# Kernel tuning notes

Measured on AMD Instinct MI355X. Metric: run time of the kernel, lower is better.

## Reference

```python
import jax, jax.numpy as jnp
import numpy as np

UP = 2
KSIZE = 3
RES = 64
LRELU_SLOPE = 0.2
ACT_GAIN = float(np.sqrt(2.0))  # def_gain of 'lrelu' in bias_act


def _setup_filter():
    # upfirdn2d.setup_filter([1,3,3,1]): normalize, make separable 2D filter
    f = jnp.array([1.0, 3.0, 3.0, 1.0], dtype=jnp.float32)
    f = f / jnp.sum(f)
    return jnp.outer(f, f)  # [4,4]


def _upfirdn2d_up2(x, f2):
    # Zero-insertion upsample by 2 + pad + FIR filter, gain = up**2.
    # Torch path: zero-insert to 2H, pad (3,2), conv 4-tap -> 2H+2.
    # lhs_dilation gives 2H-1; absorbing the trailing inserted zero into the
    # right pad ((3,3) instead of (3,2)) is exactly equivalent.
    B, C, H, W = x.shape
    k = (f2 * (UP * UP)).astype(x.dtype)[None, None]  # [1,1,4,4] (symmetric, flip-invariant)
    k = jnp.tile(k, (C, 1, 1, 1))                     # depthwise [C,1,4,4]
    return jax.lax.conv_general_dilated(
        x, k, window_strides=(1, 1), padding=((3, 3), (3, 3)),
        lhs_dilation=(UP, UP),
        dimension_numbers=('NCHW', 'OIHW', 'NCHW'),
        feature_group_count=C)


def setup_inputs() -> dict:
    key = jax.random.key(0)
    ks = jax.random.split(key, 6)
    B, Cin, Cout, Wd = 16, 512, 512, 512
    Hin = RES // UP
    return {
        "x": jax.random.normal(ks[0], (B, Cin, Hin, Hin), jnp.float32),
        "w": jax.random.normal(ks[1], (B, Wd), jnp.float32),
        "affine_weight": jax.random.normal(ks[2], (Cin, Wd), jnp.float32),
        "affine_bias": jnp.ones((Cin,), jnp.float32),  # bias_init=1
        "weight": jax.random.normal(ks[3], (Cout, Cin, KSIZE, KSIZE), jnp.float32),
        "bias": jnp.zeros((Cout,), jnp.float32),
        "noise_const": jax.random.normal(ks[4], (RES, RES), jnp.float32),
        "noise_strength": jax.random.uniform(ks[5], (), jnp.float32),
    }


def reference(x, w, affine_weight, affine_bias, weight, bias, noise_const, noise_strength):
    B, Cin, Hin, Win = x.shape
    Cout = weight.shape[0]
    # affine: FullyConnectedLayer, weight_gain = 1/sqrt(w_dim), bias_init=1
    styles = w @ affine_weight.T * (1.0 / np.sqrt(w.shape[1])) + affine_bias  # [B,Cin]
    # modulate + demodulate (fused_modconv=True): per-sample weights
    wmod = weight[None] * styles[:, None, :, None, None]                     # [B,Cout,Cin,kh,kw]
    dcoef = jax.lax.rsqrt(jnp.sum(jnp.square(wmod), axis=(2, 3, 4)) + 1e-8)  # [B,Cout]
    wmod = wmod * dcoef[:, :, None, None, None]
    # up=2 -> flip_weight=False -> true convolution: flip spatial taps
    wmod = wmod[..., ::-1, ::-1]
    # conv2d_resample: upfirdn2d upsample first (pad = k//2 + (fw+up-1)//2 = 3), then VALID conv
    xu = _upfirdn2d_up2(x, _setup_filter())                                  # [B,Cin,66,66]
    xr = xu.reshape(1, B * Cin, xu.shape[2], xu.shape[3])
    wr = wmod.reshape(B * Cout, Cin, KSIZE, KSIZE)
    y = jax.lax.conv_general_dilated(
        xr, wr, window_strides=(1, 1), padding='VALID',
        dimension_numbers=('NCHW', 'OIHW', 'NCHW'),
        feature_group_count=B)
    y = y.reshape(B, Cout, RES, RES)
    # noise_mode='const': noise = noise_const * noise_strength
    y = y + noise_const * noise_strength
    # fused bias + lrelu + def_gain (gain=1, conv_clamp=None)
    y = jax.nn.leaky_relu(y + bias[None, :, None, None], LRELU_SLOPE) * ACT_GAIN
    return y
```

## Files before the change

### kernel.cpp

```cpp
#include <hip/hip_runtime.h>
#include <hip/hip_bf16.h>
#include <math.h>

#define CIN   512
#define COUT  512
#define NB    16
#define WD    512
#define HIN   32
#define RES   64
#define LRELU 0.2f
#define ACT_GAIN 1.4142135623730951f

typedef __attribute__((ext_vector_type(8))) short short8;
typedef __attribute__((ext_vector_type(4))) float float4v;
typedef __attribute__((ext_vector_type(16))) float float16v;

__global__ void styles2_kernel(const float* __restrict__ w,
                               const float* __restrict__ aw,
                               const float* __restrict__ ab,
                               float* __restrict__ styles) {
    int b = blockIdx.x;
    int cig = blockIdx.y;
    int lane = threadIdx.x & 63, wv = threadIdx.x >> 6;
    __shared__ float wsh[WD];
    for (int e = threadIdx.x; e < WD; e += 256) wsh[e] = w[b * WD + e];
    __syncthreads();
    for (int r = 0; r < 16; ++r) {
        int ci = cig * 64 + wv * 16 + r;
        const float* arow = aw + (size_t)ci * WD;
        float acc = 0.f;
        for (int k = lane; k < WD; k += 64) acc += arow[k] * wsh[k];
        for (int off = 32; off; off >>= 1) acc += __shfl_down(acc, off, 64);
        if (lane == 0)
            styles[b * CIN + ci] = acc * 0.04419417382415922f + ab[ci];
    }
}

__global__ void prep_weights(const float* __restrict__ weight,
                             float* __restrict__ wsq,
                             __hip_bfloat16* __restrict__ gb) {
    int idx = blockIdx.x * 256 + threadIdx.x;
    int co = idx & (COUT - 1);
    int ci = idx >> 9;
    const float* wp = weight + ((size_t)co * CIN + ci) * 9;
    float wv[3][3];
    float s = 0.f;
#pragma unroll
    for (int ay = 0; ay < 3; ++ay)
#pragma unroll
        for (int ax = 0; ax < 3; ++ax) {
            float v = wp[ay * 3 + ax];
            wv[ay][ax] = v;
            s += v * v;
        }
    wsq[(size_t)co * CIN + ci] = s;

    const float cr[2][3][3] = {
        {{0.f, 0.25f, 0.75f}, {0.75f, 0.75f, 0.25f}, {0.25f, 0.f, 0.f}},
        {{0.f, 0.f, 0.25f},  {0.25f, 0.75f, 0.75f}, {0.75f, 0.25f, 0.f}}};

    int cc = ci >> 5, chi = (ci >> 3) & 3, clo = ci & 7;
#pragma unroll
    for (int phy = 0; phy < 2; ++phy) {
        float tmp[3][3];
#pragma unroll
        for (int dy = 0; dy < 3; ++dy)
#pragma unroll
            for (int ax = 0; ax < 3; ++ax)
                tmp[dy][ax] = cr[phy][dy][0] * wv[0][ax]
                            + cr[phy][dy][1] * wv[1][ax]
                            + cr[phy][dy][2] * wv[2][ax];
#pragma unroll
        for (int phx = 0; phx < 2; ++phx) {
            int ph = phy * 2 + phx;
#pragma unroll
            for (int dy = 0; dy < 3; ++dy)
#pragma unroll
                for (int dx = 0; dx < 3; ++dx) {
                    float g = tmp[dy][0] * cr[phx][dx][0]
                            + tmp[dy][1] * cr[phx][dx][1]
                            + tmp[dy][2] * cr[phx][dx][2];
                    int t = dy * 3 + dx;
                    gb[((((size_t)cc * 4 + ph) * 9 + t) * 4 + chi) * (COUT * 8)
                       + (size_t)co * 8 + clo] = __float2bfloat16(g);
                }
        }
    }
}

__global__ void dcoef2_kernel(const float* __restrict__ styles,
                              const float* __restrict__ wsq,
                              float* __restrict__ dcoef) {
    int b = blockIdx.x;
    int cog = blockIdx.y;
    int lane = threadIdx.x & 63, wv = threadIdx.x >> 6;
    __shared__ float s2[CIN];
    for (int e = threadIdx.x; e < CIN; e += 256) {
        float s = styles[b * CIN + e];
        s2[e] = s * s;
    }
    __syncthreads();
    for (int r = 0; r < 16; ++r) {
        int co = cog * 64 + wv * 16 + r;
        const float* qrow = wsq + (size_t)co * CIN;
        float acc = 0.f;
        for (int k = lane; k < CIN; k += 64) acc += qrow[k] * s2[k];
        for (int off = 32; off; off >>= 1) acc += __shfl_down(acc, off, 64);
        if (lane == 0) dcoef[b * COUT + co] = rsqrtf(acc + 1e-8f);
    }
}

__global__ void xmod_kernel(const float* __restrict__ x,
                            const float* __restrict__ styles,
                            __hip_bfloat16* __restrict__ xb) {
    __shared__ float xt[128 * 36];
    __shared__ float ssh[128];
    const int r = blockIdx.x;
    const int ci0 = blockIdx.y * 128;
    const int b = blockIdx.z;
    if (threadIdx.x < 128) ssh[threadIdx.x] = styles[b * CIN + ci0 + threadIdx.x];
    const bool inr = (r >= 1) && (r <= 32);
    if (inr) {
        for (int e = threadIdx.x; e < 1024; e += 256) {
            int ci = e >> 3, iw4 = e & 7;
            float4v v = *(const float4v*)(
                x + ((size_t)(b * CIN + ci0 + ci) * HIN + (r - 1)) * HIN + iw4 * 4);
            *(float4v*)(&xt[ci * 36 + iw4 * 4]) = v;
        }
    }
    __syncthreads();
    for (int e = threadIdx.x; e < 544; e += 256) {
        int c = e >> 4, t16 = e & 15;
        short8 sv;
#pragma unroll
        for (int u = 0; u < 8; ++u) {
            int ci = t16 * 8 + u;
            float val = 0.f;
            if (inr && c >= 1 && c <= 32) val = xt[ci * 36 + (c - 1)] * ssh[ci];
            __hip_bfloat16 h = __float2bfloat16(val);
            sv[u] = *reinterpret_cast<const short*>(&h);
        }
        *reinterpret_cast<short8*>(
            xb + (((size_t)b * 34 + r) * 34 + c) * CIN + ci0 + t16 * 8) = sv;
    }
}

#define ABUF 39936
#define BBUF 36864
#define BUFSZ (ABUF + BBUF)
#define LDS_TOT (2 * BUFSZ)

__global__ __launch_bounds__(512, 1) void conv_mfma(
        const __hip_bfloat16* __restrict__ xb,
        const __hip_bfloat16* __restrict__ gb,
        const float* __restrict__ dcoef,
        const float* __restrict__ bias,
        const float* __restrict__ noise,
        const float* __restrict__ nstr,
        float* __restrict__ out)
{
    extern __shared__ __align__(16) char smem[];
    const int tid = threadIdx.x;
    const int lane = tid & 63;
    const int wid = tid >> 6;
    const int li32 = lane & 31;
    const int hi = lane >> 5;
    const int mb = blockIdx.x;
    const int n0 = blockIdx.y * 64;
    const int bz = blockIdx.z;
    const int b  = bz >> 2;
    const int ph = bz & 3;
    const int phy = ph >> 1, phx = ph & 1;
    const int y0 = mb * 16;

    int a_goff[5];
#pragma unroll
    for (int k = 0; k < 5; ++k) {
        int n = wid + k * 8;
        int s = n * 64 + lane;
        if (s > 2447) s = 2447;
        int cr = s / 136;
        int rem = s - cr * 136;
        int chi = rem / 34;
        int col = rem - chi * 34;
        a_goff[k] = (((b * 34 + y0 + cr) * 34 + col)) * CIN + chi * 8;
    }
    int b_goff[5];
#pragma unroll
    for (int k = 0; k < 5; ++k) {
        int sl = wid + k * 8;
        b_goff[k] = (sl * COUT + n0 + lane) * 8;
    }

    float16v acc[2][2];
#pragma unroll
    for (int i = 0; i < 2; ++i)
#pragma unroll
        for (int j = 0; j < 2; ++j) acc[i][j] = (float16v)0.f;

    const char* xg = (const char*)xb;
    const char* wg = (const char*)gb;

#define STAGE(CC, BUFB) do {                                                  \
        _Pragma("unroll")                                                     \
        for (int k = 0; k < 5; ++k) {                                         \
            int sl = wid + k * 8;                                             \
            if (sl < 36) {                                                    \
                long ge = (long)b_goff[k] + (long)((CC) * 4 + ph) * 147456;   \
                __builtin_amdgcn_global_load_lds(                             \
                    (const __attribute__((address_space(1))) char*)(wg + ge * 2), \
                    (__attribute__((address_space(3))) char*)(smem + (BUFB) + ABUF + sl * 1024), \
                    16, 0, 0);                                                \
            }                                                                 \
        }                                                                     \
        _Pragma("unroll")                                                     \
        for (int k = 0; k < 5; ++k) {                                         \
            int n = wid + k * 8;                                              \
            if (n < 39) {                                                     \
                long ge = (long)(a_goff[k] + (CC) * 32);                      \
                __builtin_amdgcn_global_load_lds(                             \
                    (const __attribute__((address_space(1))) char*)(xg + ge * 2), \
                    (__attribute__((address_space(3))) char*)(smem + (BUFB) + n * 1024), \
                    16, 0, 0);                                                \
            }                                                                 \
        }                                                                     \
    } while (0)

#define LOADF(BUFB, S, SLOT) do {                                             \
        const int t_ = (S) >> 1, ks_ = (S) & 1;                               \
        const int dy1 = t_ / 3, dx1 = t_ - dy1 * 3;                           \
        _Pragma("unroll")                                                     \
        for (int nf = 0; nf < 2; ++nf)                                        \
            fB[SLOT][nf] = *(const short8*)(smem + (BUFB) + ABUF +            \
                    (((t_ * 4 + ks_ * 2 + hi) * 64) + nf * 32 + li32) * 16);  \
        _Pragma("unroll")                                                     \
        for (int mf = 0; mf < 2; ++mf)                                        \
            fA[SLOT][mf] = *(const short8*)(smem + (BUFB) +                   \
                    ((((wid * 2 + mf + dy1) * 4 + ks_ * 2 + hi) * 34) +       \
                     (li32 + dx1)) * 16);                                     \
    } while (0)

#define COMPUTE(BUFB) do {                                                    \
        short8 fA[2][2], fB[2][2];                                            \
        LOADF(BUFB, 0, 0);                                                    \
        __builtin_amdgcn_sched_group_barrier(0x100, 4, 0);    \
        __builtin_amdgcn_s_setprio(1);                                        \
        _Pragma("unroll")                                                     \
        for (int s = 0; s < 18; ++s) {                                        \
            const int cur = s & 1, nxt = cur ^ 1;                             \
            if (s < 17) LOADF(BUFB, s + 1, nxt);                              \
            _Pragma("unroll")                                                 \
            for (int mf = 0; mf < 2; ++mf)                                    \
                _Pragma("unroll")                                             \
                for (int nf = 0; nf < 2; ++nf)                                \
                    acc[mf][nf] = __builtin_amdgcn_mfma_f32_32x32x16_bf16(    \
                        fA[cur][mf], fB[cur][nf], acc[mf][nf], 0, 0, 0);      \
            if (s < 17)                                                       \
                __builtin_amdgcn_sched_group_barrier(0x100, 4, 0);  \
            __builtin_amdgcn_sched_group_barrier(0x008, 4, 0);      \
        }                                                                     \
        __builtin_amdgcn_s_setprio(0);                                        \
    } while (0)

#define SYNC() do {                                                           \
        asm volatile("s_waitcnt vmcnt(0)" ::: "memory");                      \
        __builtin_amdgcn_s_barrier();                                         \
    } while (0)

    STAGE(0, 0);
    SYNC();

#pragma unroll 1
    for (int cc = 0; cc < 16; cc += 2) {
        STAGE(cc + 1, BUFSZ);
        COMPUTE(0);
        SYNC();
        if (cc + 2 < 16) STAGE(cc + 2, 0);
        COMPUTE(BUFSZ);
        SYNC();
    }

#undef STAGE
#undef LOADF
#undef COMPUTE
#undef SYNC

    const float ns = nstr[0];
#pragma unroll
    for (int nf = 0; nf < 2; ++nf) {
        int cout = n0 + nf * 32 + li32;
        float dc = dcoef[b * COUT + cout];
        float bs = bias[cout];
#pragma unroll
        for (int mf = 0; mf < 2; ++mf) {
            int ic = y0 + wid * 2 + mf;
            int fr = 2 * ic + phy;
            float* op = out + ((size_t)(b * COUT + cout) * RES + fr) * RES;
            const float* npz = noise + fr * RES;
#pragma unroll
            for (int r2 = 0; r2 < 4; ++r2) {
#pragma unroll
                for (int u = 0; u < 4; ++u) {
                    int j = 8 * r2 + 4 * hi + u;
                    int fc = 2 * j + phx;
                    float v = acc[mf][nf][r2 * 4 + u] * dc + npz[fc] * ns + bs;
                    v = (v > 0.f ? v : LRELU * v) * ACT_GAIN;
                    op[fc] = v;
                }
            }
        }
    }
}

extern "C" void kernel_launch(void* const* d_in, const int* in_sizes, int n_in,
                              void* d_out, int out_size, void* d_ws, size_t ws_size,
                              hipStream_t stream) {
    (void)in_sizes; (void)n_in; (void)out_size; (void)ws_size;
    const float* x     = (const float*)d_in[0];
    const float* w     = (const float*)d_in[1];
    const float* aw    = (const float*)d_in[2];
    const float* ab    = (const float*)d_in[3];
    const float* wt    = (const float*)d_in[4];
    const float* bias  = (const float*)d_in[5];
    const float* noise = (const float*)d_in[6];
    const float* nstr  = (const float*)d_in[7];
    float* out = (float*)d_out;

    static bool init = false;
    if (!init) {
        hipFuncSetAttribute(reinterpret_cast<const void*>(conv_mfma),
                            hipFuncAttributeMaxDynamicSharedMemorySize, LDS_TOT);
        init = true;
    }

    char* ws = (char*)d_ws;
    float* styles = (float*)ws;
    float* dcoef  = (float*)(ws + 32768);
    float* wsq    = (float*)(ws + 65536);
    __hip_bfloat16* gb = (__hip_bfloat16*)(ws + 65536 + 1048576);
    __hip_bfloat16* xb = (__hip_bfloat16*)(ws + 65536 + 1048576 + 18874368);

    styles2_kernel<<<dim3(NB, 8), dim3(256), 0, stream>>>(w, aw, ab, styles);
    prep_weights<<<dim3(1024), dim3(256), 0, stream>>>(wt, wsq, gb);
    dcoef2_kernel<<<dim3(NB, 8), dim3(256), 0, stream>>>(styles, wsq, dcoef);
    xmod_kernel<<<dim3(34, 4, NB), dim3(256), 0, stream>>>(x, styles, xb);
    conv_mfma<<<dim3(2, 8, NB * 4), dim3(512), LDS_TOT, stream>>>(
        xb, gb, dcoef, bias, noise, nstr, out);
}
```

Measured before the change: 557.4 us.

## Interleave x-phases in weight layout for contiguous vectorized output stores

```diff
diff --git a/kernel.cpp b/kernel.cpp
--- a/kernel.cpp
+++ b/kernel.cpp
@@ -39,50 +39,65 @@
 __global__ void prep_weights(const float* __restrict__ weight,
                              float* __restrict__ wsq,
                              __hip_bfloat16* __restrict__ gb) {
-    int idx = blockIdx.x * 256 + threadIdx.x;
-    int co = idx & (COUT - 1);
-    int ci = idx >> 9;
-    const float* wp = weight + ((size_t)co * CIN + ci) * 9;
-    float wv[3][3];
-    float s = 0.f;
-#pragma unroll
-    for (int ay = 0; ay < 3; ++ay)
-#pragma unroll
-        for (int ax = 0; ax < 3; ++ax) {
-            float v = wp[ay * 3 + ax];
-            wv[ay][ax] = v;
-            s += v * v;
-        }
-    wsq[(size_t)co * CIN + ci] = s;
+    int gid = blockIdx.x * 256 + threadIdx.x;
+    int co = gid & 511;
+    int cig = gid >> 9;
+    int cc = cig >> 2, chi = cig & 3;
+    int cib = cc * 32 + chi * 8;
+    int cog = co >> 5, colo = co & 31;
+
+    float wv[8][3][3];
+#pragma unroll
+    for (int clo = 0; clo < 8; ++clo) {
+        const float* wp = weight + ((size_t)co * CIN + cib + clo) * 9;
+        float s = 0.f;
+#pragma unroll
+        for (int ay = 0; ay < 3; ++ay)
+#pragma unroll
+            for (int ax = 0; ax < 3; ++ax) {
+                float v = wp[ay * 3 + ax];
+                wv[clo][ay][ax] = v;
+                s += v * v;
+            }
+        wsq[(size_t)co * CIN + cib + clo] = s;
+    }
 
     const float cr[2][3][3] = {
         {{0.f, 0.25f, 0.75f}, {0.75f, 0.75f, 0.25f}, {0.25f, 0.f, 0.f}},
         {{0.f, 0.f, 0.25f},  {0.25f, 0.75f, 0.75f}, {0.75f, 0.25f, 0.f}}};
 
-    int cc = ci >> 5, chi = (ci >> 3) & 3, clo = ci & 7;
 #pragma unroll
     for (int phy = 0; phy < 2; ++phy) {
-        float tmp[3][3];
-#pragma unroll
-        for (int dy = 0; dy < 3; ++dy)
-#pragma unroll
-            for (int ax = 0; ax < 3; ++ax)
-                tmp[dy][ax] = cr[phy][dy][0] * wv[0][ax]
-                            + cr[phy][dy][1] * wv[1][ax]
-                            + cr[phy][dy][2] * wv[2][ax];
+        float tmp[8][3][3];
+#pragma unroll
+        for (int clo = 0; clo < 8; ++clo)
+#pragma unroll
+            for (int dy = 0; dy < 3; ++dy)
+#pragma unroll
+                for (int ax = 0; ax < 3; ++ax)
+                    tmp[clo][dy][ax] = cr[phy][dy][0] * wv[clo][0][ax]
+                                     + cr[phy][dy][1] * wv[clo][1][ax]
+                                     + cr[phy][dy][2] * wv[clo][2][ax];
 #pragma unroll
         for (int phx = 0; phx < 2; ++phx) {
-            int ph = phy * 2 + phx;
+            int n = phx * 32 + colo;
 #pragma unroll
             for (int dy = 0; dy < 3; ++dy)
 #pragma unroll
                 for (int dx = 0; dx < 3; ++dx) {
-                    float g = tmp[dy][0] * cr[phx][dx][0]
-                            + tmp[dy][1] * cr[phx][dx][1]
-                            + tmp[dy][2] * cr[phx][dx][2];
                     int t = dy * 3 + dx;
-                    gb[((((size_t)cc * 4 + ph) * 9 + t) * 4 + chi) * (COUT * 8)
-                       + (size_t)co * 8 + clo] = __float2bfloat16(g);
+                    short8 sv;
+#pragma unroll
+                    for (int clo = 0; clo < 8; ++clo) {
+                        float g = tmp[clo][dy][0] * cr[phx][dx][0]
+                                + tmp[clo][dy][1] * cr[phx][dx][1]
+                                + tmp[clo][dy][2] * cr[phx][dx][2];
+                        __hip_bfloat16 h = __float2bfloat16(g);
+                        sv[clo] = *reinterpret_cast<const short*>(&h);
+                    }
+                    size_t off = ((((((size_t)cc * 2 + phy) * 9 + t) * 4 + chi)
+                                   * 16 + cog) * 64 + n) * 8;
+                    *reinterpret_cast<short8*>(gb + off) = sv;
                 }
         }
     }
@@ -166,11 +181,10 @@
     const int li32 = lane & 31;
     const int hi = lane >> 5;
     const int mb = blockIdx.x;
-    const int n0 = blockIdx.y * 64;
+    const int cog = blockIdx.y;
     const int bz = blockIdx.z;
-    const int b  = bz >> 2;
-    const int ph = bz & 3;
-    const int phy = ph >> 1, phx = ph & 1;
+    const int b  = bz >> 1;
+    const int phy = bz & 1;
     const int y0 = mb * 16;
 
     int a_goff[5];
@@ -189,7 +203,7 @@
 #pragma unroll
     for (int k = 0; k < 5; ++k) {
         int sl = wid + k * 8;
-        b_goff[k] = (sl * COUT + n0 + lane) * 8;
+        b_goff[k] = phy * 589824 + (sl * 16 + cog) * 1024 + lane * 16;
     }
 
     float16v acc[2][2];
@@ -206,9 +220,9 @@
         for (int k = 0; k < 5; ++k) {                                         \
             int sl = wid + k * 8;                                             \
             if (sl < 36) {                                                    \
-                long ge = (long)b_goff[k] + (long)((CC) * 4 + ph) * 147456;   \
+                long ge = (long)b_goff[k] + (long)(CC) * 1179648;             \
                 __builtin_amdgcn_global_load_lds(                             \
-                    (const __attribute__((address_space(1))) char*)(wg + ge * 2), \
+                    (const __attribute__((address_space(1))) char*)(wg + ge), \
                     (__attribute__((address_space(3))) char*)(smem + (BUFB) + ABUF + sl * 1024), \
                     16, 0, 0);                                                \
             }                                                                 \
@@ -286,28 +300,33 @@
 #undef SYNC
 
     const float ns = nstr[0];
-#pragma unroll
-    for (int nf = 0; nf < 2; ++nf) {
-        int cout = n0 + nf * 32 + li32;
-        float dc = dcoef[b * COUT + cout];
-        float bs = bias[cout];
-#pragma unroll
-        for (int mf = 0; mf < 2; ++mf) {
-            int ic = y0 + wid * 2 + mf;
-            int fr = 2 * ic + phy;
-            float* op = out + ((size_t)(b * COUT + cout) * RES + fr) * RES;
-            const float* npz = noise + fr * RES;
-#pragma unroll
-            for (int r2 = 0; r2 < 4; ++r2) {
-#pragma unroll
-                for (int u = 0; u < 4; ++u) {
-                    int j = 8 * r2 + 4 * hi + u;
-                    int fc = 2 * j + phx;
-                    float v = acc[mf][nf][r2 * 4 + u] * dc + npz[fc] * ns + bs;
-                    v = (v > 0.f ? v : LRELU * v) * ACT_GAIN;
-                    op[fc] = v;
+    const int cout = cog * 32 + li32;
+    const float dc = dcoef[b * COUT + cout];
+    const float bs = bias[cout];
+#pragma unroll
+    for (int mf = 0; mf < 2; ++mf) {
+        int ic = y0 + wid * 2 + mf;
+        int fr = 2 * ic + phy;
+        float* op = out + ((size_t)(b * COUT + cout) * RES + fr) * RES;
+        const float* npz = noise + fr * RES;
+#pragma unroll
+        for (int r2 = 0; r2 < 4; ++r2) {
+            int fcb = 16 * r2 + 8 * hi;
+            float nzv[8];
+            *(float4v*)&nzv[0] = *(const float4v*)(npz + fcb);
+            *(float4v*)&nzv[4] = *(const float4v*)(npz + fcb + 4);
+            float f[8];
+#pragma unroll
+            for (int uu = 0; uu < 4; ++uu) {
+#pragma unroll
+                for (int nf = 0; nf < 2; ++nf) {
+                    float v = acc[mf][nf][r2 * 4 + uu] * dc
+                            + nzv[2 * uu + nf] * ns + bs;
+                    f[2 * uu + nf] = (v > 0.f ? v : LRELU * v) * ACT_GAIN;
                 }
             }
+            *(float4v*)(op + fcb)     = *(const float4v*)&f[0];
+            *(float4v*)(op + fcb + 4) = *(const float4v*)&f[4];
         }
     }
 }
@@ -341,9 +360,9 @@
     __hip_bfloat16* xb = (__hip_bfloat16*)(ws + 65536 + 1048576 + 18874368);
 
     styles2_kernel<<<dim3(NB, 8), dim3(256), 0, stream>>>(w, aw, ab, styles);
-    prep_weights<<<dim3(1024), dim3(256), 0, stream>>>(wt, wsq, gb);
+    prep_weights<<<dim3(128), dim3(256), 0, stream>>>(wt, wsq, gb);
     dcoef2_kernel<<<dim3(NB, 8), dim3(256), 0, stream>>>(styles, wsq, dcoef);
     xmod_kernel<<<dim3(34, 4, NB), dim3(256), 0, stream>>>(x, styles, xb);
-    conv_mfma<<<dim3(2, 8, NB * 4), dim3(512), LDS_TOT, stream>>>(
+    conv_mfma<<<dim3(2, 16, NB * 2), dim3(512), LDS_TOT, stream>>>(
         xb, gb, dcoef, bias, noise, nstr, out);
 }
```

Result: faster. 494.7 us (-11.2%).
